# Performance work log

Measured on AMD Instinct MI355X. Metric: run time of the kernel, lower is better.

Reference implementation:

```python
import jax, jax.numpy as jnp
import numpy as np

N_T = 100000   # transaction nodes
N_A = 50000    # account nodes
F = 256        # raw feature dim
H = 256        # hidden_dim
E = 800000     # edges per edge type


def setup_inputs() -> dict:
    key = jax.random.key(0)
    ks = jax.random.split(key, 14)
    s = 1.0 / np.sqrt(F)
    return {
        "x_tx": jax.random.normal(ks[0], (N_T, F), jnp.float32),
        "x_acc": jax.random.normal(ks[1], (N_A, F), jnp.float32),
        "edge_at_src": jax.random.randint(ks[2], (E,), 0, N_A, jnp.int32),
        "edge_at_dst": jax.random.randint(ks[3], (E,), 0, N_T, jnp.int32),
        "edge_ta_src": jax.random.randint(ks[4], (E,), 0, N_T, jnp.int32),
        "edge_ta_dst": jax.random.randint(ks[5], (E,), 0, N_A, jnp.int32),
        "W_l_at": jax.random.normal(ks[6], (F, H), jnp.float32) * s,
        "b_l_at": jnp.zeros((H,), jnp.float32),
        "W_r_at": jax.random.normal(ks[7], (F, H), jnp.float32) * s,
        "W_l_ta": jax.random.normal(ks[8], (F, H), jnp.float32) * s,
        "b_l_ta": jnp.zeros((H,), jnp.float32),
        "W_r_ta": jax.random.normal(ks[9], (F, H), jnp.float32) * s,
        "W_out": jax.random.normal(ks[10], (H, 1), jnp.float32) * (1.0 / np.sqrt(H)),
        "b_out": jnp.zeros((1,), jnp.float32),
    }


def _sage(x_src, x_dst, src_idx, dst_idx, W_l, b_l, W_r, num_dst):
    # PyG SAGEConv (mean aggr): lin_l(mean_j x_src[j]) + lin_r(x_dst)
    msgs = x_src[src_idx]  # [E, F] gather
    summed = jax.ops.segment_sum(msgs, dst_idx, num_segments=num_dst)  # [num_dst, F]
    cnt = jax.ops.segment_sum(jnp.ones((src_idx.shape[0],), x_src.dtype), dst_idx,
                              num_segments=num_dst)
    mean = summed / jnp.maximum(cnt, 1.0)[:, None]  # isolated dst -> zeros
    return mean @ W_l + b_l + x_dst @ W_r


def reference(x_tx, x_acc, edge_at_src, edge_at_dst, edge_ta_src, edge_ta_dst,
              W_l_at, b_l_at, W_r_at, W_l_ta, b_l_ta, W_r_ta, W_out, b_out):
    # account -> transaction SAGEConv
    h_tx = _sage(x_acc, x_tx, edge_at_src, edge_at_dst, W_l_at, b_l_at, W_r_at, N_T)
    # transaction -> account SAGEConv (computed as in HeteroConv, though unused downstream)
    h_acc = _sage(x_tx, x_acc, edge_ta_src, edge_ta_dst, W_l_ta, b_l_ta, W_r_ta, N_A)
    tx_x = jax.nn.relu(h_tx)
    _ = jax.nn.relu(h_acc)
    logits = (tx_x @ W_out + b_out)[:, 0]  # squeeze(-1)
    return logits, tx_x
```

## Files before the change

kernel.cpp:

```cpp
#include <hip/hip_runtime.h>
#include <hip/hip_bf16.h>

typedef __bf16 bf16x8_t __attribute__((ext_vector_type(8)));
typedef __bf16 bf16x4_t __attribute__((ext_vector_type(4)));
typedef float f32x4_t __attribute__((ext_vector_type(4)));

#define M_TX 100000
#define N_AC 50000
#define FDIM 256
#define HDIM 256
#define KTOT 512
#define SCAN_NBLK ((M_TX + 1023) / 1024)

__device__ inline bf16x8_t bzero8() {
    bf16x8_t v;
#pragma unroll
    for (int z = 0; z < 8; ++z) v[z] = (__bf16)0.f;
    return v;
}

__global__ __launch_bounds__(256) void initk3(float* __restrict__ logits,
                                              int* __restrict__ hist,
                                              int* __restrict__ fill,
                                              const float* __restrict__ b_out,
                                              const float* __restrict__ Wl,
                                              const float* __restrict__ Wr,
                                              __bf16* __restrict__ WT) {
    int i = blockIdx.x * 256 + threadIdx.x;
    if (i < M_TX) {
        logits[i] = b_out[0];
        hist[i] = 0;
        fill[i] = 0;
    }
    if (i < FDIM * HDIM) {
        int k = i >> 8;
        int n = i & 255;
        WT[n * KTOT + k]       = (__bf16)Wl[k * HDIM + n];
        WT[n * KTOT + 256 + k] = (__bf16)Wr[k * HDIM + n];
    }
}

__global__ __launch_bounds__(256) void cvt2k(const float* __restrict__ s1,
                                             __bf16* __restrict__ d1, int n4_1,
                                             const float* __restrict__ s2,
                                             __bf16* __restrict__ d2, int n4_2) {
    int stride = gridDim.x * 256;
    int tot = n4_1 + n4_2;
    for (int i = blockIdx.x * 256 + threadIdx.x; i < tot; i += stride) {
        const f32x4_t* sp;
        bf16x4_t* dp;
        if (i < n4_1) { sp = (const f32x4_t*)s1 + i; dp = (bf16x4_t*)d1 + i; }
        else          { sp = (const f32x4_t*)s2 + (i - n4_1); dp = (bf16x4_t*)d2 + (i - n4_1); }
        f32x4_t v = *sp;
        bf16x4_t w;
        w[0] = (__bf16)v.x; w[1] = (__bf16)v.y;
        w[2] = (__bf16)v.z; w[3] = (__bf16)v.w;
        *dp = w;
    }
}

__global__ __launch_bounds__(256) void cvtk(const float* __restrict__ src,
                                            __bf16* __restrict__ dst, int n4) {
    int stride = gridDim.x * 256;
    for (int i = blockIdx.x * 256 + threadIdx.x; i < n4; i += stride) {
        f32x4_t v = ((const f32x4_t*)src)[i];
        bf16x4_t w;
        w[0] = (__bf16)v.x; w[1] = (__bf16)v.y;
        w[2] = (__bf16)v.z; w[3] = (__bf16)v.w;
        ((bf16x4_t*)dst)[i] = w;
    }
}

__global__ __launch_bounds__(256) void histk(const int* __restrict__ edst,
                                             int* __restrict__ hist, int E) {
    int e = blockIdx.x * 256 + threadIdx.x;
    if (e >= E) return;
    atomicAdd(&hist[edst[e]], 1);
}

__global__ __launch_bounds__(1024) void scan1k(const int* __restrict__ hist,
                                               int* __restrict__ row_start,
                                               int* __restrict__ partials) {
    __shared__ int tmp[1024];
    const int b = blockIdx.x;
    const int t = threadIdx.x;
    const int i = b * 1024 + t;
    int v = (i < M_TX) ? hist[i] : 0;
    tmp[t] = v;
    __syncthreads();
    for (int off = 1; off < 1024; off <<= 1) {
        int u = (t >= off) ? tmp[t - off] : 0;
        __syncthreads();
        tmp[t] += u;
        __syncthreads();
    }
    if (i < M_TX) row_start[i] = tmp[t] - v;
    if (t == 1023) partials[b] = tmp[1023];
}

__global__ __launch_bounds__(128) void scan2k(int* __restrict__ partials,
                                              int* __restrict__ row_start) {
    __shared__ int tmp[128];
    const int t = threadIdx.x;
    int v = (t < SCAN_NBLK) ? partials[t] : 0;
    tmp[t] = v;
    __syncthreads();
    for (int off = 1; off < 128; off <<= 1) {
        int u = (t >= off) ? tmp[t - off] : 0;
        __syncthreads();
        tmp[t] += u;
        __syncthreads();
    }
    if (t < SCAN_NBLK) partials[t] = tmp[t] - v;
    if (t == 127) row_start[M_TX] = tmp[127];
}

__global__ __launch_bounds__(1024) void scan3k(int* __restrict__ row_start,
                                               const int* __restrict__ partials) {
    const int i = blockIdx.x * 1024 + threadIdx.x;
    if (i < M_TX) row_start[i] += partials[blockIdx.x];
}

__global__ __launch_bounds__(256) void scatterk(const int* __restrict__ esrc,
                                                const int* __restrict__ edst,
                                                const int* __restrict__ row_start,
                                                int* __restrict__ fill,
                                                int* __restrict__ sorted_src, int E) {
    int e = blockIdx.x * 256 + threadIdx.x;
    if (e >= E) return;
    int d = edst[e];
    int pos = row_start[d] + atomicAdd(&fill[d], 1);
    sorted_src[pos] = esrc[e];
}

__global__ __launch_bounds__(256) void gatherk(const float* __restrict__ x_acc,
                                               const __bf16* __restrict__ xab,
                                               const int* __restrict__ sorted_src,
                                               const int* __restrict__ row_start,
                                               float* __restrict__ summed,
                                               __bf16* __restrict__ meanb) {
    int gw = (blockIdx.x * 256 + threadIdx.x) >> 6;
    if (gw >= M_TX) return;
    int lane = threadIdx.x & 63;
    int start = row_start[gw];
    int end = row_start[gw + 1];
    if (xab && meanb) {
        const int l5 = lane & 31;
        const int half = lane >> 5;
        f32x4_t a0 = {0.f, 0.f, 0.f, 0.f}, a1 = {0.f, 0.f, 0.f, 0.f};
        for (int base = start; base < end; base += 64) {
            int n = end - base; if (n > 64) n = 64;
            int s = 0;
            if (base + lane < end) s = sorted_src[base + lane];
            int np = (n + 1) >> 1;
            for (int j2 = 0; j2 < np; ++j2) {
                int idx = 2 * j2 + half;
                int sj = __shfl(s, idx);
                if (idx < n) {
                    bf16x8_t v = *(const bf16x8_t*)(xab + (long)sj * FDIM + l5 * 8);
                    a0.x += (float)v[0]; a0.y += (float)v[1];
                    a0.z += (float)v[2]; a0.w += (float)v[3];
                    a1.x += (float)v[4]; a1.y += (float)v[5];
                    a1.z += (float)v[6]; a1.w += (float)v[7];
                }
            }
        }
        a0.x += __shfl_xor(a0.x, 32); a0.y += __shfl_xor(a0.y, 32);
        a0.z += __shfl_xor(a0.z, 32); a0.w += __shfl_xor(a0.w, 32);
        a1.x += __shfl_xor(a1.x, 32); a1.y += __shfl_xor(a1.y, 32);
        a1.z += __shfl_xor(a1.z, 32); a1.w += __shfl_xor(a1.w, 32);
        if (half == 0) {
            float inv = 1.0f / fmaxf((float)(end - start), 1.0f);
            bf16x8_t w;
            w[0] = (__bf16)(a0.x * inv); w[1] = (__bf16)(a0.y * inv);
            w[2] = (__bf16)(a0.z * inv); w[3] = (__bf16)(a0.w * inv);
            w[4] = (__bf16)(a1.x * inv); w[5] = (__bf16)(a1.y * inv);
            w[6] = (__bf16)(a1.z * inv); w[7] = (__bf16)(a1.w * inv);
            *(bf16x8_t*)(meanb + (long)gw * FDIM + l5 * 8) = w;
        }
        return;
    }
    f32x4_t acc = {0.f, 0.f, 0.f, 0.f};
    if (xab) {
        for (int base = start; base < end; base += 64) {
            int n = end - base; if (n > 64) n = 64;
            int s = 0;
            if (base + lane < end) s = sorted_src[base + lane];
            for (int j = 0; j < n; ++j) {
                int sj = __shfl(s, j);
                const bf16x4_t v = *(const bf16x4_t*)(xab + (long)sj * FDIM + lane * 4);
                acc.x += (float)v[0]; acc.y += (float)v[1];
                acc.z += (float)v[2]; acc.w += (float)v[3];
            }
        }
    } else {
        for (int base = start; base < end; base += 64) {
            int n = end - base; if (n > 64) n = 64;
            int s = 0;
            if (base + lane < end) s = sorted_src[base + lane];
            for (int j = 0; j < n; ++j) {
                int sj = __shfl(s, j);
                const f32x4_t v = *(const f32x4_t*)(x_acc + (long)sj * FDIM + lane * 4);
                acc.x += v.x; acc.y += v.y; acc.z += v.z; acc.w += v.w;
            }
        }
    }
    if (meanb) {
        float inv = 1.0f / fmaxf((float)(end - start), 1.0f);
        bf16x4_t w;
        w[0] = (__bf16)(acc.x * inv); w[1] = (__bf16)(acc.y * inv);
        w[2] = (__bf16)(acc.z * inv); w[3] = (__bf16)(acc.w * inv);
        *(bf16x4_t*)(meanb + (long)gw * FDIM + lane * 4) = w;
    } else {
        *(f32x4_t*)(summed + (long)gw * FDIM + lane * 4) = acc;
    }
}

__global__ __launch_bounds__(256) void gemmk2(const __bf16* __restrict__ meanb,
                                              const __bf16* __restrict__ xtb,
                                              const __bf16* __restrict__ WT,
                                              const float* __restrict__ b_l,
                                              const float* __restrict__ W_out,
                                              float* __restrict__ tx_out,
                                              float* __restrict__ logits) {
    const int tid = threadIdx.x;
    const int w = tid >> 6;
    const int lane = tid & 63;
    const int lc = lane & 15;
    const int lr = lane >> 4;
    const long m0 = (long)blockIdx.x * 64;

    f32x4_t acc[4][4];
#pragma unroll
    for (int i = 0; i < 4; ++i)
#pragma unroll
        for (int j = 0; j < 4; ++j) acc[i][j] = (f32x4_t){0.f, 0.f, 0.f, 0.f};

    long ra[4];
#pragma unroll
    for (int f = 0; f < 4; ++f) {
        long r = m0 + f * 16 + lc;
        if (r >= M_TX) r = M_TX - 1;
        ra[f] = r * FDIM;
    }
    long rb[4];
#pragma unroll
    for (int f = 0; f < 4; ++f) rb[f] = (long)(w * 64 + f * 16 + lc) * KTOT;

    const int kfr = lr * 8;
#pragma unroll
    for (int half = 0; half < 2; ++half) {
        const __bf16* Asrc = half ? xtb : meanb;
#pragma unroll 2
        for (int kt = 0; kt < 8; ++kt) {
            const int ka = kt * 32 + kfr;
            const int kb = half * 256 + kt * 32 + kfr;
            bf16x8_t af[4], bfr[4];
#pragma unroll
            for (int f = 0; f < 4; ++f) af[f] = *(const bf16x8_t*)(Asrc + ra[f] + ka);
#pragma unroll
            for (int f = 0; f < 4; ++f) bfr[f] = *(const bf16x8_t*)(WT + rb[f] + kb);
#pragma unroll
            for (int fm = 0; fm < 4; ++fm)
#pragma unroll
                for (int fn = 0; fn < 4; ++fn)
                    acc[fm][fn] = __builtin_amdgcn_mfma_f32_16x16x32_bf16(
                        af[fm], bfr[fn], acc[fm][fn], 0, 0, 0);
        }
    }

    float wout[4], bl[4];
#pragma unroll
    for (int fn = 0; fn < 4; ++fn) {
        int col = w * 64 + fn * 16 + lc;
        wout[fn] = W_out[col];
        bl[fn] = b_l[col];
    }
#pragma unroll
    for (int fm = 0; fm < 4; ++fm) {
        float part[4] = {0.f, 0.f, 0.f, 0.f};
#pragma unroll
        for (int fn = 0; fn < 4; ++fn) {
            int col = w * 64 + fn * 16 + lc;
#pragma unroll
            for (int r = 0; r < 4; ++r) {
                long row = m0 + fm * 16 + lr * 4 + r;
                float h = acc[fm][fn][r] + bl[fn];
                h = fmaxf(h, 0.0f);
                if (row < M_TX) tx_out[row * HDIM + col] = h;
                part[r] += h * wout[fn];
            }
        }
#pragma unroll
        for (int r = 0; r < 4; ++r) {
            float p = part[r];
            p += __shfl_xor(p, 1);
            p += __shfl_xor(p, 2);
            p += __shfl_xor(p, 4);
            p += __shfl_xor(p, 8);
            long row = m0 + fm * 16 + lr * 4 + r;
            if (lc == 0 && row < M_TX) unsafeAtomicAdd(logits + row, p);
        }
    }
}

__global__ __launch_bounds__(512) void gemmk(const float* __restrict__ x_tx,
                                             const float* __restrict__ summed,
                                             const int* __restrict__ row_start,
                                             const __bf16* __restrict__ WT,
                                             const float* __restrict__ b_l,
                                             const float* __restrict__ W_out,
                                             float* __restrict__ tx_out,
                                             float* __restrict__ logits) {
    __shared__ __bf16 As[128][72];
    __shared__ __bf16 Bs[256][72];

    const int m0 = blockIdx.x * 128;
    const int tid = threadIdx.x;
    const int wid = tid >> 6;
    const int lane = tid & 63;
    const int wm = wid >> 2;
    const int wn = wid & 3;
    const int lc = lane & 15;
    const int lr = lane >> 4;

    f32x4_t acc[4][4];
#pragma unroll
    for (int i = 0; i < 4; ++i)
#pragma unroll
        for (int j = 0; j < 4; ++j) acc[i][j] = (f32x4_t){0.f, 0.f, 0.f, 0.f};

    const int ar = tid >> 2;
    const int acq = tid & 3;
    const int arm = m0 + ar;
    const bool arow_ok = arm < M_TX;
    float invc;
    {
        int idx = arow_ok ? arm : (M_TX - 1);
        int c = row_start[idx + 1] - row_start[idx];
        invc = 1.0f / fmaxf((float)c, 1.0f);
    }

    for (int kc = 0; kc < 8; ++kc) {
        __syncthreads();
        {
            const bool first = kc < 4;
            const int kb = (kc & 3) * 64;
            const float sc = first ? invc : 1.0f;
            const float* base = first ? (summed + (long)arm * FDIM + kb)
                                      : (x_tx + (long)arm * FDIM + kb);
#pragma unroll
            for (int c4 = 0; c4 < 4; ++c4) {
                int kk = acq * 16 + c4 * 4;
                f32x4_t v = {0.f, 0.f, 0.f, 0.f};
                if (arow_ok) v = *(const f32x4_t*)(base + kk);
                bf16x4_t w;
                w[0] = (__bf16)(v.x * sc);
                w[1] = (__bf16)(v.y * sc);
                w[2] = (__bf16)(v.z * sc);
                w[3] = (__bf16)(v.w * sc);
                *(bf16x4_t*)(&As[ar][kk]) = w;
            }
        }
#pragma unroll
        for (int i = 0; i < 4; ++i) {
            int t2 = tid + i * 512;
            int n = t2 >> 3;
            int c = t2 & 7;
            bf16x8_t v = *(const bf16x8_t*)(WT + n * KTOT + kc * 64 + c * 8);
            *(bf16x8_t*)(&Bs[n][c * 8]) = v;
        }
        __syncthreads();
        const int kfr = lr * 8;
#pragma unroll
        for (int kk = 0; kk < 2; ++kk) {
            bf16x8_t af[4], bfr[4];
#pragma unroll
            for (int f = 0; f < 4; ++f) {
                af[f] = *(const bf16x8_t*)(&As[wm * 64 + f * 16 + lc][kk * 32 + kfr]);
                bfr[f] = *(const bf16x8_t*)(&Bs[wn * 64 + f * 16 + lc][kk * 32 + kfr]);
            }
#pragma unroll
            for (int fm = 0; fm < 4; ++fm)
#pragma unroll
                for (int fn = 0; fn < 4; ++fn)
                    acc[fm][fn] = __builtin_amdgcn_mfma_f32_16x16x32_bf16(
                        af[fm], bfr[fn], acc[fm][fn], 0, 0, 0);
        }
    }

    float wout[4], bl[4];
#pragma unroll
    for (int fn = 0; fn < 4; ++fn) {
        int col = wn * 64 + fn * 16 + lc;
        wout[fn] = W_out[col];
        bl[fn] = b_l[col];
    }
#pragma unroll
    for (int fm = 0; fm < 4; ++fm) {
        float part[4] = {0.f, 0.f, 0.f, 0.f};
#pragma unroll
        for (int fn = 0; fn < 4; ++fn) {
            int col = wn * 64 + fn * 16 + lc;
#pragma unroll
            for (int r = 0; r < 4; ++r) {
                int row = m0 + wm * 64 + fm * 16 + lr * 4 + r;
                float h = acc[fm][fn][r] + bl[fn];
                h = fmaxf(h, 0.0f);
                if (row < M_TX) tx_out[(long)row * HDIM + col] = h;
                part[r] += h * wout[fn];
            }
        }
#pragma unroll
        for (int r = 0; r < 4; ++r) {
            float p = part[r];
            p += __shfl_xor(p, 1);
            p += __shfl_xor(p, 2);
            p += __shfl_xor(p, 4);
            p += __shfl_xor(p, 8);
            int row = m0 + wm * 64 + fm * 16 + lr * 4 + r;
            if (lc == 0 && row < M_TX) unsafeAtomicAdd(logits + row, p);
        }
    }
}

extern "C" void kernel_launch(void* const* d_in, const int* in_sizes, int n_in,
                              void* d_out, int out_size, void* d_ws, size_t ws_size,
                              hipStream_t stream) {
    const float* x_tx  = (const float*)d_in[0];
    const float* x_acc = (const float*)d_in[1];
    const int* e_src   = (const int*)d_in[2];
    const int* e_dst   = (const int*)d_in[3];
    const float* W_l   = (const float*)d_in[6];
    const float* b_l   = (const float*)d_in[7];
    const float* W_r   = (const float*)d_in[8];
    const float* W_out = (const float*)d_in[12];
    const float* b_out = (const float*)d_in[13];

    float* out = (float*)d_out;
    float* logits = out;
    float* summed = out + M_TX;

    char* ws = (char*)d_ws;
    size_t off = 0;
    auto alloc = [&](size_t bytes) {
        size_t o = off;
        off = (off + bytes + 255) & ~(size_t)255;
        return o;
    };
    size_t o_WT       = alloc((size_t)HDIM * KTOT * 2);
    size_t o_rowstart = alloc(((size_t)M_TX + 1) * 4);
    size_t o_fill     = alloc((size_t)M_TX * 4);
    size_t o_sorted   = alloc((size_t)800000 * 4);
    size_t o_hist     = alloc((size_t)M_TX * 4);
    size_t o_part     = alloc((size_t)SCAN_NBLK * 4);
    size_t o_xa       = alloc((size_t)N_AC * FDIM * 2);
    size_t lvlA_end   = off;
    size_t o_mean     = alloc((size_t)M_TX * FDIM * 2);
    size_t lvlB_end   = off;
    size_t o_xt       = alloc((size_t)M_TX * FDIM * 2);
    size_t lvlC_end   = off;

    __bf16* WT       = (__bf16*)(ws + o_WT);
    int* row_start   = (int*)(ws + o_rowstart);
    int* fill        = (int*)(ws + o_fill);
    int* sorted_src  = (int*)(ws + o_sorted);
    int* histp       = (int*)(ws + o_hist);
    int* partials    = (int*)(ws + o_part);

    const bool lvlA = ws_size >= lvlA_end;
    const bool lvlB = ws_size >= lvlB_end;
    const bool lvlC = ws_size >= lvlC_end;
    __bf16* xab   = lvlA ? (__bf16*)(ws + o_xa)   : nullptr;
    __bf16* meanb = lvlB ? (__bf16*)(ws + o_mean) : nullptr;
    __bf16* xtb   = lvlC ? (__bf16*)(ws + o_xt)   : nullptr;

    const int E = in_sizes[2];

    hipLaunchKernelGGL(initk3, dim3((M_TX + 255) / 256), dim3(256), 0, stream,
                       logits, histp, fill, b_out, W_l, W_r, WT);
    if (xab && xtb)
        hipLaunchKernelGGL(cvt2k, dim3(2048), dim3(256), 0, stream,
                           x_acc, xab, N_AC * FDIM / 4, x_tx, xtb, M_TX * FDIM / 4);
    else if (xab)
        hipLaunchKernelGGL(cvtk, dim3(2048), dim3(256), 0, stream,
                           x_acc, xab, N_AC * FDIM / 4);
    hipLaunchKernelGGL(histk, dim3((E + 255) / 256), dim3(256), 0, stream,
                       e_dst, histp, E);
    hipLaunchKernelGGL(scan1k, dim3(SCAN_NBLK), dim3(1024), 0, stream,
                       histp, row_start, partials);
    hipLaunchKernelGGL(scan2k, dim3(1), dim3(128), 0, stream, partials, row_start);
    hipLaunchKernelGGL(scan3k, dim3(SCAN_NBLK), dim3(1024), 0, stream,
                       row_start, partials);
    hipLaunchKernelGGL(scatterk, dim3((E + 255) / 256), dim3(256), 0, stream,
                       e_src, e_dst, row_start, fill, sorted_src, E);
    hipLaunchKernelGGL(gatherk, dim3(M_TX / 4), dim3(256), 0, stream,
                       x_acc, xab, sorted_src, row_start, summed, meanb);
    if (meanb && xtb)
        hipLaunchKernelGGL(gemmk2, dim3((M_TX + 63) / 64), dim3(256), 0, stream,
                           meanb, xtb, WT, b_l, W_out, out + M_TX, logits);
    else
        hipLaunchKernelGGL(gemmk, dim3((M_TX + 127) / 128), dim3(512), 0, stream,
                           x_tx, summed, row_start, WT, b_l, W_out, out + M_TX, logits);
}
```

Baseline: 502.6 us.

## Fuse neighbor mean gather into GEMM via LDS, drop bf16 x_tx pre-conversion

The separate gather kernel and bf16 mean buffer are replaced by one fused kernel. Each 128-row block first gathers and averages neighbor features into shared memory, then runs the GEMM reading the mean half from LDS and converting x_tx fp32 to bf16 on the fly. The global round trip of the mean matrix and the full x_tx conversion pass are removed. In exchange, shared memory use grows to about 120 KB per block, which lowers occupancy. The gather phase and the GEMM phase also cannot overlap within a block.

```diff
diff --git a/kernel.cpp b/kernel.cpp
--- a/kernel.cpp
+++ b/kernel.cpp
@@ -11,13 +11,6 @@
 #define HDIM 256
 #define KTOT 512
 #define SCAN_NBLK ((M_TX + 1023) / 1024)
-
-__device__ inline bf16x8_t bzero8() {
-    bf16x8_t v;
-#pragma unroll
-    for (int z = 0; z < 8; ++z) v[z] = (__bf16)0.f;
-    return v;
-}
 
 __global__ __launch_bounds__(256) void initk3(float* __restrict__ logits,
                                               int* __restrict__ hist,
@@ -40,25 +33,6 @@
     }
 }
 
-__global__ __launch_bounds__(256) void cvt2k(const float* __restrict__ s1,
-                                             __bf16* __restrict__ d1, int n4_1,
-                                             const float* __restrict__ s2,
-                                             __bf16* __restrict__ d2, int n4_2) {
-    int stride = gridDim.x * 256;
-    int tot = n4_1 + n4_2;
-    for (int i = blockIdx.x * 256 + threadIdx.x; i < tot; i += stride) {
-        const f32x4_t* sp;
-        bf16x4_t* dp;
-        if (i < n4_1) { sp = (const f32x4_t*)s1 + i; dp = (bf16x4_t*)d1 + i; }
-        else          { sp = (const f32x4_t*)s2 + (i - n4_1); dp = (bf16x4_t*)d2 + (i - n4_1); }
-        f32x4_t v = *sp;
-        bf16x4_t w;
-        w[0] = (__bf16)v.x; w[1] = (__bf16)v.y;
-        w[2] = (__bf16)v.z; w[3] = (__bf16)v.w;
-        *dp = w;
-    }
-}
-
 __global__ __launch_bounds__(256) void cvtk(const float* __restrict__ src,
                                             __bf16* __restrict__ dst, int n4) {
     int stride = gridDim.x * 256;
@@ -133,102 +107,74 @@
     sorted_src[pos] = esrc[e];
 }
 
-__global__ __launch_bounds__(256) void gatherk(const float* __restrict__ x_acc,
-                                               const __bf16* __restrict__ xab,
-                                               const int* __restrict__ sorted_src,
-                                               const int* __restrict__ row_start,
-                                               float* __restrict__ summed,
-                                               __bf16* __restrict__ meanb) {
-    int gw = (blockIdx.x * 256 + threadIdx.x) >> 6;
-    if (gw >= M_TX) return;
-    int lane = threadIdx.x & 63;
-    int start = row_start[gw];
-    int end = row_start[gw + 1];
-    if (xab && meanb) {
-        const int l5 = lane & 31;
-        const int half = lane >> 5;
-        f32x4_t a0 = {0.f, 0.f, 0.f, 0.f}, a1 = {0.f, 0.f, 0.f, 0.f};
-        for (int base = start; base < end; base += 64) {
-            int n = end - base; if (n > 64) n = 64;
-            int s = 0;
-            if (base + lane < end) s = sorted_src[base + lane];
-            int np = (n + 1) >> 1;
-            for (int j2 = 0; j2 < np; ++j2) {
-                int idx = 2 * j2 + half;
-                int sj = __shfl(s, idx);
-                if (idx < n) {
-                    bf16x8_t v = *(const bf16x8_t*)(xab + (long)sj * FDIM + l5 * 8);
-                    a0.x += (float)v[0]; a0.y += (float)v[1];
-                    a0.z += (float)v[2]; a0.w += (float)v[3];
-                    a1.x += (float)v[4]; a1.y += (float)v[5];
-                    a1.z += (float)v[6]; a1.w += (float)v[7];
-                }
-            }
-        }
-        a0.x += __shfl_xor(a0.x, 32); a0.y += __shfl_xor(a0.y, 32);
-        a0.z += __shfl_xor(a0.z, 32); a0.w += __shfl_xor(a0.w, 32);
-        a1.x += __shfl_xor(a1.x, 32); a1.y += __shfl_xor(a1.y, 32);
-        a1.z += __shfl_xor(a1.z, 32); a1.w += __shfl_xor(a1.w, 32);
-        if (half == 0) {
-            float inv = 1.0f / fmaxf((float)(end - start), 1.0f);
-            bf16x8_t w;
-            w[0] = (__bf16)(a0.x * inv); w[1] = (__bf16)(a0.y * inv);
-            w[2] = (__bf16)(a0.z * inv); w[3] = (__bf16)(a0.w * inv);
-            w[4] = (__bf16)(a1.x * inv); w[5] = (__bf16)(a1.y * inv);
-            w[6] = (__bf16)(a1.z * inv); w[7] = (__bf16)(a1.w * inv);
-            *(bf16x8_t*)(meanb + (long)gw * FDIM + l5 * 8) = w;
-        }
-        return;
-    }
-    f32x4_t acc = {0.f, 0.f, 0.f, 0.f};
-    if (xab) {
-        for (int base = start; base < end; base += 64) {
-            int n = end - base; if (n > 64) n = 64;
-            int s = 0;
-            if (base + lane < end) s = sorted_src[base + lane];
-            for (int j = 0; j < n; ++j) {
-                int sj = __shfl(s, j);
-                const bf16x4_t v = *(const bf16x4_t*)(xab + (long)sj * FDIM + lane * 4);
-                acc.x += (float)v[0]; acc.y += (float)v[1];
-                acc.z += (float)v[2]; acc.w += (float)v[3];
-            }
-        }
-    } else {
-        for (int base = start; base < end; base += 64) {
-            int n = end - base; if (n > 64) n = 64;
-            int s = 0;
-            if (base + lane < end) s = sorted_src[base + lane];
-            for (int j = 0; j < n; ++j) {
-                int sj = __shfl(s, j);
-                const f32x4_t v = *(const f32x4_t*)(x_acc + (long)sj * FDIM + lane * 4);
-                acc.x += v.x; acc.y += v.y; acc.z += v.z; acc.w += v.w;
-            }
-        }
-    }
-    if (meanb) {
-        float inv = 1.0f / fmaxf((float)(end - start), 1.0f);
-        bf16x4_t w;
-        w[0] = (__bf16)(acc.x * inv); w[1] = (__bf16)(acc.y * inv);
-        w[2] = (__bf16)(acc.z * inv); w[3] = (__bf16)(acc.w * inv);
-        *(bf16x4_t*)(meanb + (long)gw * FDIM + lane * 4) = w;
-    } else {
-        *(f32x4_t*)(summed + (long)gw * FDIM + lane * 4) = acc;
-    }
-}
-
-__global__ __launch_bounds__(256) void gemmk2(const __bf16* __restrict__ meanb,
-                                              const __bf16* __restrict__ xtb,
+__global__ __launch_bounds__(512) void fusedk(const float* __restrict__ x_tx,
+                                              const __bf16* __restrict__ xab,
+                                              const int* __restrict__ sorted_src,
+                                              const int* __restrict__ row_start,
                                               const __bf16* __restrict__ WT,
                                               const float* __restrict__ b_l,
                                               const float* __restrict__ W_out,
                                               float* __restrict__ tx_out,
                                               float* __restrict__ logits) {
+    __shared__ __bf16 meanLds[128][264];
+    __shared__ __bf16 As[128][72];
+    __shared__ __bf16 Bs[256][72];
+
+    const int m0 = blockIdx.x * 128;
     const int tid = threadIdx.x;
     const int w = tid >> 6;
     const int lane = tid & 63;
+
+    {
+        const int l5 = lane & 31;
+        const int half = lane >> 5;
+        for (int rr = 0; rr < 16; ++rr) {
+            const int lrow = w * 16 + rr;
+            const int row = m0 + lrow;
+            f32x4_t a0 = {0.f, 0.f, 0.f, 0.f}, a1 = {0.f, 0.f, 0.f, 0.f};
+            int deg = 0;
+            if (row < M_TX) {
+                int start = row_start[row];
+                int end = row_start[row + 1];
+                deg = end - start;
+                for (int base = start; base < end; base += 64) {
+                    int n = end - base; if (n > 64) n = 64;
+                    int s = 0;
+                    if (base + lane < end) s = sorted_src[base + lane];
+                    int np = (n + 1) >> 1;
+                    for (int j2 = 0; j2 < np; ++j2) {
+                        int idx = 2 * j2 + half;
+                        int sj = __shfl(s, idx);
+                        if (idx < n) {
+                            bf16x8_t v = *(const bf16x8_t*)(xab + (long)sj * FDIM + l5 * 8);
+                            a0.x += (float)v[0]; a0.y += (float)v[1];
+                            a0.z += (float)v[2]; a0.w += (float)v[3];
+                            a1.x += (float)v[4]; a1.y += (float)v[5];
+                            a1.z += (float)v[6]; a1.w += (float)v[7];
+                        }
+                    }
+                }
+            }
+            a0.x += __shfl_xor(a0.x, 32); a0.y += __shfl_xor(a0.y, 32);
+            a0.z += __shfl_xor(a0.z, 32); a0.w += __shfl_xor(a0.w, 32);
+            a1.x += __shfl_xor(a1.x, 32); a1.y += __shfl_xor(a1.y, 32);
+            a1.z += __shfl_xor(a1.z, 32); a1.w += __shfl_xor(a1.w, 32);
+            if (half == 0) {
+                float inv = 1.0f / fmaxf((float)deg, 1.0f);
+                bf16x8_t wv;
+                wv[0] = (__bf16)(a0.x * inv); wv[1] = (__bf16)(a0.y * inv);
+                wv[2] = (__bf16)(a0.z * inv); wv[3] = (__bf16)(a0.w * inv);
+                wv[4] = (__bf16)(a1.x * inv); wv[5] = (__bf16)(a1.y * inv);
+                wv[6] = (__bf16)(a1.z * inv); wv[7] = (__bf16)(a1.w * inv);
+                *(bf16x8_t*)(&meanLds[lrow][l5 * 8]) = wv;
+            }
+        }
+    }
+
+    const int wm = w >> 2;
+    const int wn = w & 3;
     const int lc = lane & 15;
     const int lr = lane >> 4;
-    const long m0 = (long)blockIdx.x * 64;
 
     f32x4_t acc[4][4];
 #pragma unroll
@@ -236,30 +182,52 @@
 #pragma unroll
         for (int j = 0; j < 4; ++j) acc[i][j] = (f32x4_t){0.f, 0.f, 0.f, 0.f};
 
-    long ra[4];
-#pragma unroll
-    for (int f = 0; f < 4; ++f) {
-        long r = m0 + f * 16 + lc;
-        if (r >= M_TX) r = M_TX - 1;
-        ra[f] = r * FDIM;
-    }
-    long rb[4];
-#pragma unroll
-    for (int f = 0; f < 4; ++f) rb[f] = (long)(w * 64 + f * 16 + lc) * KTOT;
-
-    const int kfr = lr * 8;
-#pragma unroll
-    for (int half = 0; half < 2; ++half) {
-        const __bf16* Asrc = half ? xtb : meanb;
-#pragma unroll 2
-        for (int kt = 0; kt < 8; ++kt) {
-            const int ka = kt * 32 + kfr;
-            const int kb = half * 256 + kt * 32 + kfr;
+    const int ar = tid >> 2;
+    const int acq = tid & 3;
+    const int arm = m0 + ar;
+    const bool arow_ok = arm < M_TX;
+
+    for (int kc = 0; kc < 8; ++kc) {
+        __syncthreads();
+        if (kc >= 4) {
+            const int kb = (kc & 3) * 64;
+            const float* base = x_tx + (long)arm * FDIM + kb;
+#pragma unroll
+            for (int c4 = 0; c4 < 4; ++c4) {
+                int kk = acq * 16 + c4 * 4;
+                f32x4_t v = {0.f, 0.f, 0.f, 0.f};
+                if (arow_ok) v = *(const f32x4_t*)(base + kk);
+                bf16x4_t wv;
+                wv[0] = (__bf16)v.x; wv[1] = (__bf16)v.y;
+                wv[2] = (__bf16)v.z; wv[3] = (__bf16)v.w;
+                *(bf16x4_t*)(&As[ar][kk]) = wv;
+            }
+        }
+#pragma unroll
+        for (int i = 0; i < 4; ++i) {
+            int t2 = tid + i * 512;
+            int n = t2 >> 3;
+            int c = t2 & 7;
+            bf16x8_t v = *(const bf16x8_t*)(WT + n * KTOT + kc * 64 + c * 8);
+            *(bf16x8_t*)(&Bs[n][c * 8]) = v;
+        }
+        __syncthreads();
+        const int kfr = lr * 8;
+#pragma unroll
+        for (int kk = 0; kk < 2; ++kk) {
             bf16x8_t af[4], bfr[4];
-#pragma unroll
-            for (int f = 0; f < 4; ++f) af[f] = *(const bf16x8_t*)(Asrc + ra[f] + ka);
-#pragma unroll
-            for (int f = 0; f < 4; ++f) bfr[f] = *(const bf16x8_t*)(WT + rb[f] + kb);
+            if (kc < 4) {
+#pragma unroll
+                for (int f = 0; f < 4; ++f)
+                    af[f] = *(const bf16x8_t*)(&meanLds[wm * 64 + f * 16 + lc][kc * 64 + kk * 32 + kfr]);
+            } else {
+#pragma unroll
+                for (int f = 0; f < 4; ++f)
+                    af[f] = *(const bf16x8_t*)(&As[wm * 64 + f * 16 + lc][kk * 32 + kfr]);
+            }
+#pragma unroll
+            for (int f = 0; f < 4; ++f)
+                bfr[f] = *(const bf16x8_t*)(&Bs[wn * 64 + f * 16 + lc][kk * 32 + kfr]);
 #pragma unroll
             for (int fm = 0; fm < 4; ++fm)
 #pragma unroll
@@ -272,7 +240,7 @@
     float wout[4], bl[4];
 #pragma unroll
     for (int fn = 0; fn < 4; ++fn) {
-        int col = w * 64 + fn * 16 + lc;
+        int col = wn * 64 + fn * 16 + lc;
         wout[fn] = W_out[col];
         bl[fn] = b_l[col];
     }
@@ -281,13 +249,13 @@
         float part[4] = {0.f, 0.f, 0.f, 0.f};
 #pragma unroll
         for (int fn = 0; fn < 4; ++fn) {
-            int col = w * 64 + fn * 16 + lc;
+            int col = wn * 64 + fn * 16 + lc;
 #pragma unroll
             for (int r = 0; r < 4; ++r) {
-                long row = m0 + fm * 16 + lr * 4 + r;
+                int row = m0 + wm * 64 + fm * 16 + lr * 4 + r;
                 float h = acc[fm][fn][r] + bl[fn];
                 h = fmaxf(h, 0.0f);
-                if (row < M_TX) tx_out[row * HDIM + col] = h;
+                if (row < M_TX) tx_out[(long)row * HDIM + col] = h;
                 part[r] += h * wout[fn];
             }
         }
@@ -298,20 +266,43 @@
             p += __shfl_xor(p, 2);
             p += __shfl_xor(p, 4);
             p += __shfl_xor(p, 8);
-            long row = m0 + fm * 16 + lr * 4 + r;
+            int row = m0 + wm * 64 + fm * 16 + lr * 4 + r;
             if (lc == 0 && row < M_TX) unsafeAtomicAdd(logits + row, p);
         }
     }
 }
 
-__global__ __launch_bounds__(512) void gemmk(const float* __restrict__ x_tx,
-                                             const float* __restrict__ summed,
-                                             const int* __restrict__ row_start,
-                                             const __bf16* __restrict__ WT,
-                                             const float* __restrict__ b_l,
-                                             const float* __restrict__ W_out,
-                                             float* __restrict__ tx_out,
-                                             float* __restrict__ logits) {
+__global__ __launch_bounds__(256) void gatherk_f32(const float* __restrict__ x_acc,
+                                                   const int* __restrict__ sorted_src,
+                                                   const int* __restrict__ row_start,
+                                                   float* __restrict__ summed) {
+    int gw = (blockIdx.x * 256 + threadIdx.x) >> 6;
+    if (gw >= M_TX) return;
+    int lane = threadIdx.x & 63;
+    int start = row_start[gw];
+    int end = row_start[gw + 1];
+    f32x4_t acc = {0.f, 0.f, 0.f, 0.f};
+    for (int base = start; base < end; base += 64) {
+        int n = end - base; if (n > 64) n = 64;
+        int s = 0;
+        if (base + lane < end) s = sorted_src[base + lane];
+        for (int j = 0; j < n; ++j) {
+            int sj = __shfl(s, j);
+            const f32x4_t v = *(const f32x4_t*)(x_acc + (long)sj * FDIM + lane * 4);
+            acc.x += v.x; acc.y += v.y; acc.z += v.z; acc.w += v.w;
+        }
+    }
+    *(f32x4_t*)(summed + (long)gw * FDIM + lane * 4) = acc;
+}
+
+__global__ __launch_bounds__(512) void gemmk_fb(const float* __restrict__ x_tx,
+                                                const float* __restrict__ summed,
+                                                const int* __restrict__ row_start,
+                                                const __bf16* __restrict__ WT,
+                                                const float* __restrict__ b_l,
+                                                const float* __restrict__ W_out,
+                                                float* __restrict__ tx_out,
+                                                float* __restrict__ logits) {
     __shared__ __bf16 As[128][72];
     __shared__ __bf16 Bs[256][72];
 
@@ -354,12 +345,12 @@
                 int kk = acq * 16 + c4 * 4;
                 f32x4_t v = {0.f, 0.f, 0.f, 0.f};
                 if (arow_ok) v = *(const f32x4_t*)(base + kk);
-                bf16x4_t w;
-                w[0] = (__bf16)(v.x * sc);
-                w[1] = (__bf16)(v.y * sc);
-                w[2] = (__bf16)(v.z * sc);
-                w[3] = (__bf16)(v.w * sc);
-                *(bf16x4_t*)(&As[ar][kk]) = w;
+                bf16x4_t wv;
+                wv[0] = (__bf16)(v.x * sc);
+                wv[1] = (__bf16)(v.y * sc);
+                wv[2] = (__bf16)(v.z * sc);
+                wv[3] = (__bf16)(v.w * sc);
+                *(bf16x4_t*)(&As[ar][kk]) = wv;
             }
         }
 #pragma unroll
@@ -456,10 +447,6 @@
     size_t o_part     = alloc((size_t)SCAN_NBLK * 4);
     size_t o_xa       = alloc((size_t)N_AC * FDIM * 2);
     size_t lvlA_end   = off;
-    size_t o_mean     = alloc((size_t)M_TX * FDIM * 2);
-    size_t lvlB_end   = off;
-    size_t o_xt       = alloc((size_t)M_TX * FDIM * 2);
-    size_t lvlC_end   = off;
 
     __bf16* WT       = (__bf16*)(ws + o_WT);
     int* row_start   = (int*)(ws + o_rowstart);
@@ -469,20 +456,13 @@
     int* partials    = (int*)(ws + o_part);
 
     const bool lvlA = ws_size >= lvlA_end;
-    const bool lvlB = ws_size >= lvlB_end;
-    const bool lvlC = ws_size >= lvlC_end;
-    __bf16* xab   = lvlA ? (__bf16*)(ws + o_xa)   : nullptr;
-    __bf16* meanb = lvlB ? (__bf16*)(ws + o_mean) : nullptr;
-    __bf16* xtb   = lvlC ? (__bf16*)(ws + o_xt)   : nullptr;
+    __bf16* xab = lvlA ? (__bf16*)(ws + o_xa) : nullptr;
 
     const int E = in_sizes[2];
 
     hipLaunchKernelGGL(initk3, dim3((M_TX + 255) / 256), dim3(256), 0, stream,
                        logits, histp, fill, b_out, W_l, W_r, WT);
-    if (xab && xtb)
-        hipLaunchKernelGGL(cvt2k, dim3(2048), dim3(256), 0, stream,
-                           x_acc, xab, N_AC * FDIM / 4, x_tx, xtb, M_TX * FDIM / 4);
-    else if (xab)
+    if (xab)
         hipLaunchKernelGGL(cvtk, dim3(2048), dim3(256), 0, stream,
                            x_acc, xab, N_AC * FDIM / 4);
     hipLaunchKernelGGL(histk, dim3((E + 255) / 256), dim3(256), 0, stream,
@@ -494,12 +474,14 @@
                        row_start, partials);
     hipLaunchKernelGGL(scatterk, dim3((E + 255) / 256), dim3(256), 0, stream,
                        e_src, e_dst, row_start, fill, sorted_src, E);
-    hipLaunchKernelGGL(gatherk, dim3(M_TX / 4), dim3(256), 0, stream,
-                       x_acc, xab, sorted_src, row_start, summed, meanb);
-    if (meanb && xtb)
-        hipLaunchKernelGGL(gemmk2, dim3((M_TX + 63) / 64), dim3(256), 0, stream,
-                           meanb, xtb, WT, b_l, W_out, out + M_TX, logits);
-    else
-        hipLaunchKernelGGL(gemmk, dim3((M_TX + 127) / 128), dim3(512), 0, stream,
+    if (xab) {
+        hipLaunchKernelGGL(fusedk, dim3((M_TX + 127) / 128), dim3(512), 0, stream,
+                           x_tx, xab, sorted_src, row_start, WT, b_l, W_out,
+                           out + M_TX, logits);
+    } else {
+        hipLaunchKernelGGL(gatherk_f32, dim3(M_TX / 4), dim3(256), 0, stream,
+                           x_acc, sorted_src, row_start, summed);
+        hipLaunchKernelGGL(gemmk_fb, dim3((M_TX + 127) / 128), dim3(512), 0, stream,
                            x_tx, summed, row_start, WT, b_l, W_out, out + M_TX, logits);
-}
+    }
+}
```

After: 521.8 us. 3.8% more time.
